# Performance work log

Hardware: AMD Instinct MI355X
Metric: run time of the kernel (lower is better)

The kernel has to match this reference:

```python
import jax, jax.numpy as jnp
import numpy as np

T, B, H, L = 1024, 64, 512, 2
IN = 512  # input_size == hidden_size so layer weights stack
GATE = 3 * H  # fixed-forget subLSTM: in_gate, out_gate, z


def setup_inputs() -> dict:
    key = jax.random.key(0)
    ks = jax.random.split(key, 6)
    stdv = 1.0 / np.sqrt(H)
    u = lambda k, shape: jax.random.uniform(k, shape, jnp.float32, -stdv, stdv)
    return {
        "x": jax.random.normal(ks[0], (T, B, IN), jnp.float32),
        "h0": jnp.zeros((L, B, H), jnp.float32),
        "c0": jnp.zeros((L, B, H), jnp.float32),
        "W": u(ks[1], (L, GATE, IN)),
        "R": u(ks[2], (L, GATE, H)),
        "bi": u(ks[3], (L, GATE)),
        "bh": u(ks[4], (L, GATE)),
        "f": u(ks[5], (L, H)),
    }


def reference(x, h0, c0, W, R, bi, bh, f):
    num_layers = W.shape[0]
    fg = jax.nn.sigmoid(f)  # fixed forget gate per layer/unit, [L, H]

    def step(carry, x_t):
        h, c = carry  # each [L, B, H]
        inp = x_t  # [B, IN]
        new_h, new_c = [], []
        for l in range(num_layers):
            proj = jax.nn.sigmoid(inp @ W[l].T + bi[l] + h[l] @ R[l].T + bh[l])
            i_g, o_g, z = jnp.split(proj, 3, axis=-1)
            c_t = c[l] * fg[l] + z - i_g
            h_t = jax.nn.sigmoid(c_t) - o_g
            new_h.append(h_t)
            new_c.append(c_t)
            inp = h_t
        return (jnp.stack(new_h), jnp.stack(new_c)), inp

    (h_f, c_f), output = jax.lax.scan(step, (h0, c0), x)
    return output, h_f, c_f
```

## Files before the change

kernel.cpp:

```cpp
#include <hip/hip_runtime.h>
#include <hip/hip_bf16.h>
#include <stdint.h>


#define TSTEPS 1024
#define BATCH  64
#define HID    512
#define GATE   1536
#define GROWS  8
#define NT     256
#define NBLOCKS 256

typedef unsigned long long u64;
typedef __attribute__((ext_vector_type(8))) short short8;
typedef __attribute__((ext_vector_type(4))) short short4v;
typedef __attribute__((ext_vector_type(4))) float floatx4;

__device__ __forceinline__ float sigmoidf_(float x) { return 1.0f / (1.0f + __expf(-x)); }

__device__ __forceinline__ unsigned short f2bf(float x) {
    union { float f; unsigned u; } v; v.f = x;
    unsigned r = v.u + 0x7FFFu + ((v.u >> 16) & 1u);
    return (unsigned short)(r >> 16);
}

__device__ __forceinline__ short8 load_frag(const float* p) {
    floatx4 a = *(const floatx4*)p;
    floatx4 b = *(const floatx4*)(p + 4);
    short8 r;
#pragma unroll
    for (int j = 0; j < 4; ++j) { r[j] = (short)f2bf(a[j]); r[j+4] = (short)f2bf(b[j]); }
    return r;
}

__device__ __forceinline__ u64 ring_ld(const u64* p) {
    return __hip_atomic_load(p, __ATOMIC_RELAXED, __HIP_MEMORY_SCOPE_AGENT);
}
__device__ __forceinline__ void ring_st(u64* p, u64 v) {
    __hip_atomic_store(p, v, __ATOMIC_RELAXED, __HIP_MEMORY_SCOPE_AGENT);
}

__global__ __launch_bounds__(256) void xconvert(const float* __restrict__ x,
                                                unsigned short* __restrict__ xb) {
    const size_t i = ((size_t)blockIdx.x*256 + threadIdx.x) * 8;
    floatx4 a = *(const floatx4*)(x + i);
    floatx4 b = *(const floatx4*)(x + i + 4);
    short8 p;
#pragma unroll
    for (int j = 0; j < 4; ++j) { p[j] = (short)f2bf(a[j]); p[j+4] = (short)f2bf(b[j]); }
    *(short8*)(xb + i) = p;
}

__global__ __launch_bounds__(NT, 1) void sublstm_fused(
    const unsigned short* __restrict__ xb,
    const float* __restrict__ W,
    const float* __restrict__ R,
    const float* __restrict__ bi,
    const float* __restrict__ bh,
    const float* __restrict__ fw,
    const float* __restrict__ h0,
    const float* __restrict__ c0,
    u64* __restrict__ ring,
    float* __restrict__ out)
{
    const int tid  = threadIdx.x;
    const int lane = tid & 63;
    const int wid  = tid >> 6;
    const int bid  = blockIdx.x;
    const int g    = bid & 7;
    const int bidx = bid >> 3;
    const int col0 = bidx << 4;

    __shared__ __align__(16) unsigned short x_tile[16][520];
    __shared__ __align__(16) unsigned short hA[16][520];
    __shared__ __align__(16) unsigned short hB[16][520];
    __shared__ float proj[3][16][17];

    for (int i = tid; i < 16*520; i += NT) {
        ((unsigned short*)x_tile)[i] = 0;
        ((unsigned short*)hA)[i] = 0;
        ((unsigned short*)hB)[i] = 0;
    }
    __syncthreads();

    const int lrow = lane & 15;
    const int lk   = (lane >> 4) << 3;

    short8 wf0[16], rf0[16], wf1[16], rf1[16];
    float bias0 = 0.f, bias1 = 0.f;
    if (wid < 3) {
        const int wrow = wid*HID + col0 + lrow;
#pragma unroll
        for (int kc = 0; kc < 16; ++kc) {
            wf0[kc] = load_frag(W + (size_t)wrow*HID + kc*32 + lk);
            rf0[kc] = load_frag(R + (size_t)wrow*HID + kc*32 + lk);
            wf1[kc] = load_frag(W + ((size_t)GATE + wrow)*HID + kc*32 + lk);
            rf1[kc] = load_frag(R + ((size_t)GATE + wrow)*HID + kc*32 + lk);
        }
        bias0 = bi[wrow] + bh[wrow];
        bias1 = bi[GATE + wrow] + bh[GATE + wrow];
    }

    const int lyr  = tid >> 7;
    const int srow = (tid >> 4) & 7;
    const int scol = tid & 15;
    const float fgv = sigmoidf_(fw[(size_t)lyr*HID + col0 + scol]);
    float creg = c0[((size_t)lyr*BATCH + g*GROWS + srow)*HID + col0 + scol];

    {
        const unsigned short* xp = xb + (size_t)g*GROWS*HID;
        for (int w = tid; w < GROWS*HID/8; w += NT) {
            const int r = w >> 6, c8 = (w & 63) << 3;
            *(short8*)(&x_tile[r][c8]) = *(const short8*)(xp + (size_t)r*HID + c8);
        }
        const float* hp0 = h0 + (size_t)g*GROWS*HID;
        const float* hp1 = h0 + ((size_t)BATCH + g*GROWS)*HID;
        for (int w = tid; w < GROWS*HID/4; w += NT) {
            const int r = w >> 7, c4 = (w & 127) << 2;
            floatx4 va_ = *(const floatx4*)(hp0 + (size_t)r*HID + c4);
            floatx4 vb_ = *(const floatx4*)(hp1 + (size_t)r*HID + c4);
            short4v pa, pb;
#pragma unroll
            for (int j = 0; j < 4; ++j) { pa[j] = (short)f2bf(va_[j]); pb[j] = (short)f2bf(vb_[j]); }
            *(short4v*)(&hA[r][c4]) = pa;
            *(short4v*)(&hB[r][c4]) = pb;
        }
    }
    __syncthreads();

    int budget = 1 << 22;
    int pend_t = -1;
    float pend_h = 0.f, pend_c = 0.f;
    u64 va0[8], va1[8];
    short8 xr0, xr1;

    for (int i = 0; i <= TSTEPS; ++i) {
        if (i >= 1) {
            const unsigned want = (unsigned)i;
            const u64* rb0 = ring + ((size_t)((i - 1) & 3)*8 + g)*2048;
            unsigned stale = 0;
#pragma unroll
            for (int k = 0; k < 8; ++k)
                if ((unsigned)(va0[k] >> 32) != want) stale |= (1u << k);
            int pass = 0;
            while (__any((int)(stale != 0)) && budget > 0) {
                if (pass++) __builtin_amdgcn_s_sleep(1);
#pragma unroll
                for (int k = 0; k < 8; ++k)
                    if (stale & (1u << k)) va0[k] = ring_ld(rb0 + tid + (k << 8));
#pragma unroll
                for (int k = 0; k < 8; ++k)
                    if (stale & (1u << k))
                        if ((unsigned)(va0[k] >> 32) == want) stale &= ~(1u << k);
                --budget;
            }
#pragma unroll
            for (int k = 0; k < 8; ++k) {
                const int w = tid + (k << 8);
                const int b = w >> 6, r = (w >> 3) & 7, u = w & 7;
                *(unsigned*)(&hA[r][b*16 + u*2]) = (unsigned)va0[k];
            }
            if (i < TSTEPS) {
                *(short8*)(&x_tile[tid >> 6][(tid & 63) << 3]) = xr0;
                const int w1 = tid + 256;
                *(short8*)(&x_tile[w1 >> 6][(w1 & 63) << 3]) = xr1;
            }
        }
        __syncthreads();

        if (wid < 3 && i < TSTEPS) {
            floatx4 a0a = {0,0,0,0}, a0b = {0,0,0,0};
#pragma unroll
            for (int kc = 0; kc < 16; ++kc) {
                short8 afx = *(const short8*)(&x_tile[lrow][kc*32 + lk]);
                short8 afh = *(const short8*)(&hA[lrow][kc*32 + lk]);
                a0a = __builtin_amdgcn_mfma_f32_16x16x32_bf16(afx, wf0[kc], a0a, 0, 0, 0);
                a0b = __builtin_amdgcn_mfma_f32_16x16x32_bf16(afh, rf0[kc], a0b, 0, 0, 0);
            }
            const int erow0 = (lane >> 4) << 2, ecol = lrow;
#pragma unroll
            for (int q = 0; q < 4; ++q)
                proj[wid][erow0 + q][ecol] = sigmoidf_(a0a[q] + a0b[q] + bias0);
        }
        __syncthreads();

        if (i >= 2) {
            const u64* rb1 = ring + ((size_t)(4 + ((i - 2) & 3))*8 + g)*2048;
#pragma unroll
            for (int k = 0; k < 8; ++k)
                va1[k] = ring_ld(rb1 + tid + (k << 8));
        }
        __builtin_amdgcn_sched_barrier(0);

        if (pend_t >= 0) {
            if (lyr == 1)
                out[((size_t)pend_t*BATCH + g*GROWS + srow)*HID + col0 + scol] = pend_h;
            if (pend_t == TSTEPS - 1) {
                const size_t fo = (size_t)TSTEPS*BATCH*HID
                                + ((size_t)lyr*BATCH + g*GROWS + srow)*HID + col0 + scol;
                out[fo] = pend_h;
                out[fo + (size_t)2*BATCH*HID] = pend_c;
            }
            pend_t = -1;
        }
        if (lyr == 0 && i < TSTEPS) {
            const float ig = proj[0][srow][scol];
            const float og = proj[1][srow][scol];
            const float zz = proj[2][srow][scol];
            const float c_ = creg*fgv + zz - ig;
            creg = c_;
            const float h_ = sigmoidf_(c_) - og;
            const unsigned hu = __float_as_uint(h_);
            const unsigned pu = (unsigned)__builtin_amdgcn_ds_swizzle((int)hu, 0x041F);
            unsigned pay;
            asm volatile("v_cvt_pk_bf16_f32 %0, %1, %2"
                         : "=v"(pay) : "v"(h_), "v"(__uint_as_float(pu)));
            if (!(scol & 1)) {
                const size_t off = (((size_t)(i & 3)*8 + g)*32 + bidx)*64
                                 + srow*8 + (scol >> 1);
                ring_st(ring + off, (u64)pay | ((u64)(unsigned)(i + 1) << 32));
            }
            if (i == TSTEPS - 1) { pend_t = i; pend_h = h_; pend_c = c_; }
        }
        __builtin_amdgcn_sched_barrier(0);

        floatx4 a1a = {0,0,0,0};
        if (wid < 3 && i >= 1) {
#pragma unroll
            for (int kc = 0; kc < 16; ++kc) {
                short8 afh = *(const short8*)(&hA[lrow][kc*32 + lk]);
                a1a = __builtin_amdgcn_mfma_f32_16x16x32_bf16(afh, wf1[kc], a1a, 0, 0, 0);
            }
        }
        __builtin_amdgcn_sched_barrier(0);

        if (i >= 2) {
            const unsigned want = (unsigned)(i - 1);
            const u64* rb1 = ring + ((size_t)(4 + ((i - 2) & 3))*8 + g)*2048;
            unsigned stale = 0;
#pragma unroll
            for (int k = 0; k < 8; ++k)
                if ((unsigned)(va1[k] >> 32) != want) stale |= (1u << k);
            int pass = 0;
            while (__any((int)(stale != 0)) && budget > 0) {
                if (pass++) __builtin_amdgcn_s_sleep(1);
#pragma unroll
                for (int k = 0; k < 8; ++k)
                    if (stale & (1u << k)) va1[k] = ring_ld(rb1 + tid + (k << 8));
#pragma unroll
                for (int k = 0; k < 8; ++k)
                    if (stale & (1u << k))
                        if ((unsigned)(va1[k] >> 32) == want) stale &= ~(1u << k);
                --budget;
            }
#pragma unroll
            for (int k = 0; k < 8; ++k) {
                const int w = tid + (k << 8);
                const int b = w >> 6, r = (w >> 3) & 7, u = w & 7;
                *(unsigned*)(&hB[r][b*16 + u*2]) = (unsigned)va1[k];
            }
        }
        __syncthreads();

        if (wid < 3 && i >= 1) {
            floatx4 a1b = {0,0,0,0};
#pragma unroll
            for (int kc = 0; kc < 16; ++kc) {
                short8 afb = *(const short8*)(&hB[lrow][kc*32 + lk]);
                a1b = __builtin_amdgcn_mfma_f32_16x16x32_bf16(afb, rf1[kc], a1b, 0, 0, 0);
            }
            const int erow0 = (lane >> 4) << 2, ecol = lrow;
#pragma unroll
            for (int q = 0; q < 4; ++q)
                proj[wid][erow0 + q][ecol] = sigmoidf_(a1a[q] + a1b[q] + bias1);
        }
        __syncthreads();

        if (i < TSTEPS) {
            const u64* rb0n = ring + ((size_t)(i & 3)*8 + g)*2048;
#pragma unroll
            for (int k = 0; k < 8; ++k)
                va0[k] = ring_ld(rb0n + tid + (k << 8));
        }
        if (i + 1 < TSTEPS) {
            const unsigned short* xp = xb + ((size_t)(i + 1)*BATCH + g*GROWS)*HID;
            xr0 = *(const short8*)(xp + (size_t)(tid >> 6)*HID + ((tid & 63) << 3));
            const int w1 = tid + 256;
            xr1 = *(const short8*)(xp + (size_t)(w1 >> 6)*HID + ((w1 & 63) << 3));
        }
        __builtin_amdgcn_sched_barrier(0);

        if (lyr == 1 && i >= 1) {
            const int t = i - 1;
            const float ig = proj[0][srow][scol];
            const float og = proj[1][srow][scol];
            const float zz = proj[2][srow][scol];
            const float c_ = creg*fgv + zz - ig;
            creg = c_;
            const float h_ = sigmoidf_(c_) - og;
            const unsigned hu = __float_as_uint(h_);
            const unsigned pu = (unsigned)__builtin_amdgcn_ds_swizzle((int)hu, 0x041F);
            unsigned pay;
            asm volatile("v_cvt_pk_bf16_f32 %0, %1, %2"
                         : "=v"(pay) : "v"(h_), "v"(__uint_as_float(pu)));
            if (!(scol & 1)) {
                const size_t off = (((size_t)(4 + (t & 3))*8 + g)*32 + bidx)*64
                                 + srow*8 + (scol >> 1);
                ring_st(ring + off, (u64)pay | ((u64)(unsigned)(t + 1) << 32));
            }
            pend_t = t; pend_h = h_; pend_c = c_;
        }
    }

    if (pend_t >= 0) {
        if (lyr == 1)
            out[((size_t)pend_t*BATCH + g*GROWS + srow)*HID + col0 + scol] = pend_h;
        if (pend_t == TSTEPS - 1) {
            const size_t fo = (size_t)TSTEPS*BATCH*HID
                            + ((size_t)lyr*BATCH + g*GROWS + srow)*HID + col0 + scol;
            out[fo] = pend_h;
            out[fo + (size_t)2*BATCH*HID] = pend_c;
        }
    }
}

extern "C" void kernel_launch(void* const* d_in, const int* in_sizes, int n_in,
                              void* d_out, int out_size, void* d_ws, size_t ws_size,
                              hipStream_t stream)
{
    (void)in_sizes; (void)n_in; (void)out_size; (void)ws_size;
    const float* x  = (const float*)d_in[0];
    const float* h0 = (const float*)d_in[1];
    const float* c0 = (const float*)d_in[2];
    const float* W  = (const float*)d_in[3];
    const float* R  = (const float*)d_in[4];
    const float* bi = (const float*)d_in[5];
    const float* bh = (const float*)d_in[6];
    const float* fw = (const float*)d_in[7];
    float* out = (float*)d_out;

    u64* ring = (u64*)d_ws;
    unsigned short* xbuf = (unsigned short*)((char*)d_ws + (2u << 20));

    hipMemsetAsync(d_ws, 0, (size_t)2*4*8*2048*8, stream);

    xconvert<<<dim3(TSTEPS*BATCH*HID/(256*8)), dim3(256), 0, stream>>>(x, xbuf);

    sublstm_fused<<<dim3(NBLOCKS), dim3(NT), 0, stream>>>(
        xbuf, W, R, bi, bh, fw, h0, c0, ring, out);
}
```

Measured before the change: 3.467 ms.

## Precompute next-step input projection off the critical path and split MFMA accumulators

The layer-0 input projection x_t·W is now computed one step ahead, at the end of the previous iteration, and kept in registers, so the recurrent critical section only runs the h·R MFMAs. The x tile is prefetched two steps ahead. The recurrent MFMA chains are split into two independent accumulators to hide MFMA dependency latency. Output stores and ring loads are moved into slack between barriers. This adds register pressure and reorders the x_tile writes relative to barriers, which could race if the sync placement is wrong.

```diff
diff --git a/kernel.cpp b/kernel.cpp
--- a/kernel.cpp
+++ b/kernel.cpp
@@ -128,11 +128,26 @@
     }
     __syncthreads();
 
+    floatx4 a0a_sav = {0,0,0,0};
+    if (wid < 3) {
+#pragma unroll
+        for (int kc = 0; kc < 16; ++kc) {
+            short8 afx = *(const short8*)(&x_tile[lrow][kc*32 + lk]);
+            a0a_sav = __builtin_amdgcn_mfma_f32_16x16x32_bf16(afx, wf0[kc], a0a_sav, 0, 0, 0);
+        }
+    }
+    short8 xr0, xr1;
+    {
+        const unsigned short* xp = xb + (size_t)BATCH*HID + (size_t)g*GROWS*HID;
+        xr0 = *(const short8*)(xp + (size_t)(tid >> 6)*HID + ((tid & 63) << 3));
+        const int w1 = tid + 256;
+        xr1 = *(const short8*)(xp + (size_t)(w1 >> 6)*HID + ((w1 & 63) << 3));
+    }
+
     int budget = 1 << 22;
     int pend_t = -1;
     float pend_h = 0.f, pend_c = 0.f;
     u64 va0[8], va1[8];
-    short8 xr0, xr1;
 
     for (int i = 0; i <= TSTEPS; ++i) {
         if (i >= 1) {
@@ -160,27 +175,22 @@
                 const int b = w >> 6, r = (w >> 3) & 7, u = w & 7;
                 *(unsigned*)(&hA[r][b*16 + u*2]) = (unsigned)va0[k];
             }
-            if (i < TSTEPS) {
-                *(short8*)(&x_tile[tid >> 6][(tid & 63) << 3]) = xr0;
-                const int w1 = tid + 256;
-                *(short8*)(&x_tile[w1 >> 6][(w1 & 63) << 3]) = xr1;
-            }
         }
         __syncthreads();
 
         if (wid < 3 && i < TSTEPS) {
-            floatx4 a0a = {0,0,0,0}, a0b = {0,0,0,0};
-#pragma unroll
-            for (int kc = 0; kc < 16; ++kc) {
-                short8 afx = *(const short8*)(&x_tile[lrow][kc*32 + lk]);
-                short8 afh = *(const short8*)(&hA[lrow][kc*32 + lk]);
-                a0a = __builtin_amdgcn_mfma_f32_16x16x32_bf16(afx, wf0[kc], a0a, 0, 0, 0);
-                a0b = __builtin_amdgcn_mfma_f32_16x16x32_bf16(afh, rf0[kc], a0b, 0, 0, 0);
+            floatx4 ae = {0,0,0,0}, ao = {0,0,0,0};
+#pragma unroll
+            for (int kc = 0; kc < 16; kc += 2) {
+                short8 h0f = *(const short8*)(&hA[lrow][kc*32 + lk]);
+                short8 h1f = *(const short8*)(&hA[lrow][(kc+1)*32 + lk]);
+                ae = __builtin_amdgcn_mfma_f32_16x16x32_bf16(h0f, rf0[kc],   ae, 0, 0, 0);
+                ao = __builtin_amdgcn_mfma_f32_16x16x32_bf16(h1f, rf0[kc+1], ao, 0, 0, 0);
             }
             const int erow0 = (lane >> 4) << 2, ecol = lrow;
 #pragma unroll
             for (int q = 0; q < 4; ++q)
-                proj[wid][erow0 + q][ecol] = sigmoidf_(a0a[q] + a0b[q] + bias0);
+                proj[wid][erow0 + q][ecol] = sigmoidf_(a0a_sav[q] + ae[q] + ao[q] + bias0);
         }
         __syncthreads();
 
@@ -192,17 +202,6 @@
         }
         __builtin_amdgcn_sched_barrier(0);
 
-        if (pend_t >= 0) {
-            if (lyr == 1)
-                out[((size_t)pend_t*BATCH + g*GROWS + srow)*HID + col0 + scol] = pend_h;
-            if (pend_t == TSTEPS - 1) {
-                const size_t fo = (size_t)TSTEPS*BATCH*HID
-                                + ((size_t)lyr*BATCH + g*GROWS + srow)*HID + col0 + scol;
-                out[fo] = pend_h;
-                out[fo + (size_t)2*BATCH*HID] = pend_c;
-            }
-            pend_t = -1;
-        }
         if (lyr == 0 && i < TSTEPS) {
             const float ig = proj[0][srow][scol];
             const float og = proj[1][srow][scol];
@@ -260,35 +259,51 @@
                 *(unsigned*)(&hB[r][b*16 + u*2]) = (unsigned)va1[k];
             }
         }
-        __syncthreads();
-
-        if (wid < 3 && i >= 1) {
-            floatx4 a1b = {0,0,0,0};
-#pragma unroll
-            for (int kc = 0; kc < 16; ++kc) {
-                short8 afb = *(const short8*)(&hB[lrow][kc*32 + lk]);
-                a1b = __builtin_amdgcn_mfma_f32_16x16x32_bf16(afb, rf1[kc], a1b, 0, 0, 0);
-            }
-            const int erow0 = (lane >> 4) << 2, ecol = lrow;
-#pragma unroll
-            for (int q = 0; q < 4; ++q)
-                proj[wid][erow0 + q][ecol] = sigmoidf_(a1a[q] + a1b[q] + bias1);
-        }
-        __syncthreads();
-
-        if (i < TSTEPS) {
-            const u64* rb0n = ring + ((size_t)(i & 3)*8 + g)*2048;
-#pragma unroll
-            for (int k = 0; k < 8; ++k)
-                va0[k] = ring_ld(rb0n + tid + (k << 8));
-        }
         if (i + 1 < TSTEPS) {
-            const unsigned short* xp = xb + ((size_t)(i + 1)*BATCH + g*GROWS)*HID;
+            *(short8*)(&x_tile[tid >> 6][(tid & 63) << 3]) = xr0;
+            const int w1 = tid + 256;
+            *(short8*)(&x_tile[w1 >> 6][(w1 & 63) << 3]) = xr1;
+        }
+        if (i + 2 < TSTEPS) {
+            const unsigned short* xp = xb + ((size_t)(i + 2)*BATCH + g*GROWS)*HID;
             xr0 = *(const short8*)(xp + (size_t)(tid >> 6)*HID + ((tid & 63) << 3));
             const int w1 = tid + 256;
             xr1 = *(const short8*)(xp + (size_t)(w1 >> 6)*HID + ((w1 & 63) << 3));
         }
-        __builtin_amdgcn_sched_barrier(0);
+        if (pend_t >= 0) {
+            if (lyr == 1)
+                out[((size_t)pend_t*BATCH + g*GROWS + srow)*HID + col0 + scol] = pend_h;
+            if (pend_t == TSTEPS - 1) {
+                const size_t fo = (size_t)TSTEPS*BATCH*HID
+                                + ((size_t)lyr*BATCH + g*GROWS + srow)*HID + col0 + scol;
+                out[fo] = pend_h;
+                out[fo + (size_t)2*BATCH*HID] = pend_c;
+            }
+            pend_t = -1;
+        }
+        __syncthreads();
+
+        if (wid < 3 && i >= 1) {
+            floatx4 be = {0,0,0,0}, bo = {0,0,0,0};
+#pragma unroll
+            for (int kc = 0; kc < 16; kc += 2) {
+                short8 b0f = *(const short8*)(&hB[lrow][kc*32 + lk]);
+                short8 b1f = *(const short8*)(&hB[lrow][(kc+1)*32 + lk]);
+                be = __builtin_amdgcn_mfma_f32_16x16x32_bf16(b0f, rf1[kc],   be, 0, 0, 0);
+                bo = __builtin_amdgcn_mfma_f32_16x16x32_bf16(b1f, rf1[kc+1], bo, 0, 0, 0);
+            }
+            const int erow0 = (lane >> 4) << 2, ecol = lrow;
+#pragma unroll
+            for (int q = 0; q < 4; ++q)
+                proj[wid][erow0 + q][ecol] = sigmoidf_(a1a[q] + be[q] + bo[q] + bias1);
+        }
+        if (i < TSTEPS) {
+            const u64* rb0n = ring + ((size_t)(i & 3)*8 + g)*2048;
+#pragma unroll
+            for (int k = 0; k < 8; ++k)
+                va0[k] = ring_ld(rb0n + tid + (k << 8));
+        }
+        __syncthreads();
 
         if (lyr == 1 && i >= 1) {
             const int t = i - 1;
@@ -310,6 +325,16 @@
             }
             pend_t = t; pend_h = h_; pend_c = c_;
         }
+
+        if (wid < 3 && i + 1 < TSTEPS) {
+            floatx4 an = {0,0,0,0};
+#pragma unroll
+            for (int kc = 0; kc < 16; ++kc) {
+                short8 afx = *(const short8*)(&x_tile[lrow][kc*32 + lk]);
+                an = __builtin_amdgcn_mfma_f32_16x16x32_bf16(afx, wf0[kc], an, 0, 0, 0);
+            }
+            a0a_sav = an;
+        }
     }
 
     if (pend_t >= 0) {
```

Measured after the change: 3.429 ms. No clear change (-1.1%).

## Halve block count with 32 columns per block and six MFMA waves

Applied to the files above, without the earlier changes.

Each block now owns 32 hidden columns instead of 16 and runs six waves, all of which do MFMA work, instead of four waves with one idle. This halves the number of persistent blocks, so fewer producers write to the ring buffer and the per-step barriers cover fewer participants. The layer-1 ring reload and the output stores are moved to overlap with other work, and x-prefetch now happens earlier. In exchange each block carries more weight fragments in registers and does more elementwise work, which lengthens the serial per-step path inside a block.

```diff
diff --git a/kernel.cpp b/kernel.cpp
--- a/kernel.cpp
+++ b/kernel.cpp
@@ -8,8 +8,10 @@
 #define HID    512
 #define GATE   1536
 #define GROWS  8
-#define NT     256
-#define NBLOCKS 256
+#define NT     384
+#define NBLOCKS 128
+#define BPG    16
+#define GWORDS 2048
 
 typedef unsigned long long u64;
 typedef __attribute__((ext_vector_type(8))) short short8;
@@ -69,12 +71,12 @@
     const int bid  = blockIdx.x;
     const int g    = bid & 7;
     const int bidx = bid >> 3;
-    const int col0 = bidx << 4;
+    const int col0 = bidx << 5;
 
     __shared__ __align__(16) unsigned short x_tile[16][520];
     __shared__ __align__(16) unsigned short hA[16][520];
     __shared__ __align__(16) unsigned short hB[16][520];
-    __shared__ float proj[3][16][17];
+    __shared__ float proj[3][16][33];
 
     for (int i = tid; i < 16*520; i += NT) {
         ((unsigned short*)x_tile)[i] = 0;
@@ -88,8 +90,8 @@
 
     short8 wf0[16], rf0[16], wf1[16], rf1[16];
     float bias0 = 0.f, bias1 = 0.f;
-    if (wid < 3) {
-        const int wrow = wid*HID + col0 + lrow;
+    {
+        const int wrow = (wid >> 1)*HID + col0 + (wid & 1)*16 + lrow;
 #pragma unroll
         for (int kc = 0; kc < 16; ++kc) {
             wf0[kc] = load_frag(W + (size_t)wrow*HID + kc*32 + lk);
@@ -101,11 +103,20 @@
         bias1 = bi[GATE + wrow] + bh[GATE + wrow];
     }
 
-    const int lyr  = tid >> 7;
-    const int srow = (tid >> 4) & 7;
-    const int scol = tid & 15;
-    const float fgv = sigmoidf_(fw[(size_t)lyr*HID + col0 + scol]);
-    float creg = c0[((size_t)lyr*BATCH + g*GROWS + srow)*HID + col0 + scol];
+    const bool hasL0 = (tid < 256);
+    const bool hasL1 = (tid >= 128);
+    const int c0i = tid, c1i = tid - 128;
+    const int sr0 = (c0i >> 5) & 7, sc0 = c0i & 31;
+    const int sr1 = (c1i >> 5) & 7, sc1 = c1i & 31;
+    float fgv0 = 0.f, fgv1 = 0.f, creg0 = 0.f, creg1 = 0.f;
+    if (hasL0) {
+        fgv0 = sigmoidf_(fw[col0 + sc0]);
+        creg0 = c0[((size_t)g*GROWS + sr0)*HID + col0 + sc0];
+    }
+    if (hasL1) {
+        fgv1 = sigmoidf_(fw[(size_t)HID + col0 + sc1]);
+        creg1 = c0[((size_t)BATCH + g*GROWS + sr1)*HID + col0 + sc1];
+    }
 
     {
         const unsigned short* xp = xb + (size_t)g*GROWS*HID;
@@ -131,44 +142,66 @@
     int budget = 1 << 22;
     int pend_t = -1;
     float pend_h = 0.f, pend_c = 0.f;
-    u64 va0[8], va1[8];
+    u64 va0[6], va1[6];
     short8 xr0, xr1;
+    {
+        const unsigned short* xp = xb + (size_t)BATCH*HID + (size_t)g*GROWS*HID;
+        xr0 = *(const short8*)(xp + (size_t)(tid >> 6)*HID + ((tid & 63) << 3));
+        if (tid < 128) {
+            const int w1 = tid + NT;
+            xr1 = *(const short8*)(xp + (size_t)(w1 >> 6)*HID + ((w1 & 63) << 3));
+        }
+    }
 
     for (int i = 0; i <= TSTEPS; ++i) {
         if (i >= 1) {
             const unsigned want = (unsigned)i;
-            const u64* rb0 = ring + ((size_t)((i - 1) & 3)*8 + g)*2048;
+            const u64* rb0 = ring + ((size_t)((i - 1) & 3)*8 + g)*GWORDS;
             unsigned stale = 0;
 #pragma unroll
-            for (int k = 0; k < 8; ++k)
-                if ((unsigned)(va0[k] >> 32) != want) stale |= (1u << k);
+            for (int k = 0; k < 6; ++k) {
+                const int w = tid + k*NT;
+                if (w < GWORDS && (unsigned)(va0[k] >> 32) != want) stale |= (1u << k);
+            }
             int pass = 0;
             while (__any((int)(stale != 0)) && budget > 0) {
                 if (pass++) __builtin_amdgcn_s_sleep(1);
 #pragma unroll
-                for (int k = 0; k < 8; ++k)
-                    if (stale & (1u << k)) va0[k] = ring_ld(rb0 + tid + (k << 8));
-#pragma unroll
-                for (int k = 0; k < 8; ++k)
+                for (int k = 0; k < 6; ++k)
+                    if (stale & (1u << k)) va0[k] = ring_ld(rb0 + tid + k*NT);
+#pragma unroll
+                for (int k = 0; k < 6; ++k)
                     if (stale & (1u << k))
                         if ((unsigned)(va0[k] >> 32) == want) stale &= ~(1u << k);
                 --budget;
             }
 #pragma unroll
-            for (int k = 0; k < 8; ++k) {
-                const int w = tid + (k << 8);
-                const int b = w >> 6, r = (w >> 3) & 7, u = w & 7;
-                *(unsigned*)(&hA[r][b*16 + u*2]) = (unsigned)va0[k];
+            for (int k = 0; k < 6; ++k) {
+                const int w = tid + k*NT;
+                if (w < GWORDS) {
+                    const int b = w >> 7, r = (w >> 4) & 7, u = w & 15;
+                    *(unsigned*)(&hA[r][b*32 + u*2]) = (unsigned)va0[k];
+                }
             }
             if (i < TSTEPS) {
                 *(short8*)(&x_tile[tid >> 6][(tid & 63) << 3]) = xr0;
-                const int w1 = tid + 256;
-                *(short8*)(&x_tile[w1 >> 6][(w1 & 63) << 3]) = xr1;
+                if (tid < 128) {
+                    const int w1 = tid + NT;
+                    *(short8*)(&x_tile[w1 >> 6][(w1 & 63) << 3]) = xr1;
+                }
+            }
+        }
+        if (i + 1 < TSTEPS) {
+            const unsigned short* xp = xb + ((size_t)(i + 1)*BATCH + g*GROWS)*HID;
+            xr0 = *(const short8*)(xp + (size_t)(tid >> 6)*HID + ((tid & 63) << 3));
+            if (tid < 128) {
+                const int w1 = tid + NT;
+                xr1 = *(const short8*)(xp + (size_t)(w1 >> 6)*HID + ((w1 & 63) << 3));
             }
         }
         __syncthreads();
 
-        if (wid < 3 && i < TSTEPS) {
+        if (i < TSTEPS) {
             floatx4 a0a = {0,0,0,0}, a0b = {0,0,0,0};
 #pragma unroll
             for (int kc = 0; kc < 16; ++kc) {
@@ -177,55 +210,51 @@
                 a0a = __builtin_amdgcn_mfma_f32_16x16x32_bf16(afx, wf0[kc], a0a, 0, 0, 0);
                 a0b = __builtin_amdgcn_mfma_f32_16x16x32_bf16(afh, rf0[kc], a0b, 0, 0, 0);
             }
-            const int erow0 = (lane >> 4) << 2, ecol = lrow;
+            const int erow0 = (lane >> 4) << 2, ecol = (wid & 1)*16 + lrow;
 #pragma unroll
             for (int q = 0; q < 4; ++q)
-                proj[wid][erow0 + q][ecol] = sigmoidf_(a0a[q] + a0b[q] + bias0);
+                proj[wid >> 1][erow0 + q][ecol] = sigmoidf_(a0a[q] + a0b[q] + bias0);
         }
         __syncthreads();
 
         if (i >= 2) {
-            const u64* rb1 = ring + ((size_t)(4 + ((i - 2) & 3))*8 + g)*2048;
-#pragma unroll
-            for (int k = 0; k < 8; ++k)
-                va1[k] = ring_ld(rb1 + tid + (k << 8));
+            const u64* rb1 = ring + (size_t)4*8*GWORDS + ((size_t)((i - 2) & 3)*8 + g)*GWORDS;
+#pragma unroll
+            for (int k = 0; k < 6; ++k) {
+                const int w = tid + k*NT;
+                if (w < GWORDS) va1[k] = ring_ld(rb1 + w);
+            }
         }
         __builtin_amdgcn_sched_barrier(0);
 
-        if (pend_t >= 0) {
-            if (lyr == 1)
-                out[((size_t)pend_t*BATCH + g*GROWS + srow)*HID + col0 + scol] = pend_h;
-            if (pend_t == TSTEPS - 1) {
-                const size_t fo = (size_t)TSTEPS*BATCH*HID
-                                + ((size_t)lyr*BATCH + g*GROWS + srow)*HID + col0 + scol;
-                out[fo] = pend_h;
-                out[fo + (size_t)2*BATCH*HID] = pend_c;
-            }
-            pend_t = -1;
-        }
-        if (lyr == 0 && i < TSTEPS) {
-            const float ig = proj[0][srow][scol];
-            const float og = proj[1][srow][scol];
-            const float zz = proj[2][srow][scol];
-            const float c_ = creg*fgv + zz - ig;
-            creg = c_;
+        if (hasL0 && i < TSTEPS) {
+            const float ig = proj[0][sr0][sc0];
+            const float og = proj[1][sr0][sc0];
+            const float zz = proj[2][sr0][sc0];
+            const float c_ = creg0*fgv0 + zz - ig;
+            creg0 = c_;
             const float h_ = sigmoidf_(c_) - og;
             const unsigned hu = __float_as_uint(h_);
             const unsigned pu = (unsigned)__builtin_amdgcn_ds_swizzle((int)hu, 0x041F);
             unsigned pay;
             asm volatile("v_cvt_pk_bf16_f32 %0, %1, %2"
                          : "=v"(pay) : "v"(h_), "v"(__uint_as_float(pu)));
-            if (!(scol & 1)) {
-                const size_t off = (((size_t)(i & 3)*8 + g)*32 + bidx)*64
-                                 + srow*8 + (scol >> 1);
+            if (!(sc0 & 1)) {
+                const size_t off = (((size_t)(i & 3)*8 + g)*BPG + bidx)*128
+                                 + sr0*16 + (sc0 >> 1);
                 ring_st(ring + off, (u64)pay | ((u64)(unsigned)(i + 1) << 32));
             }
-            if (i == TSTEPS - 1) { pend_t = i; pend_h = h_; pend_c = c_; }
+            if (i == TSTEPS - 1) {
+                const size_t fo = (size_t)TSTEPS*BATCH*HID
+                                + ((size_t)g*GROWS + sr0)*HID + col0 + sc0;
+                out[fo] = h_;
+                out[fo + (size_t)2*BATCH*HID] = creg0;
+            }
         }
         __builtin_amdgcn_sched_barrier(0);
 
         floatx4 a1a = {0,0,0,0};
-        if (wid < 3 && i >= 1) {
+        if (i >= 1) {
 #pragma unroll
             for (int kc = 0; kc < 16; ++kc) {
                 short8 afh = *(const short8*)(&hA[lrow][kc*32 + lk]);
@@ -236,76 +265,85 @@
 
         if (i >= 2) {
             const unsigned want = (unsigned)(i - 1);
-            const u64* rb1 = ring + ((size_t)(4 + ((i - 2) & 3))*8 + g)*2048;
+            const u64* rb1 = ring + (size_t)4*8*GWORDS + ((size_t)((i - 2) & 3)*8 + g)*GWORDS;
             unsigned stale = 0;
 #pragma unroll
-            for (int k = 0; k < 8; ++k)
-                if ((unsigned)(va1[k] >> 32) != want) stale |= (1u << k);
+            for (int k = 0; k < 6; ++k) {
+                const int w = tid + k*NT;
+                if (w < GWORDS && (unsigned)(va1[k] >> 32) != want) stale |= (1u << k);
+            }
             int pass = 0;
             while (__any((int)(stale != 0)) && budget > 0) {
                 if (pass++) __builtin_amdgcn_s_sleep(1);
 #pragma unroll
-                for (int k = 0; k < 8; ++k)
-                    if (stale & (1u << k)) va1[k] = ring_ld(rb1 + tid + (k << 8));
-#pragma unroll
-                for (int k = 0; k < 8; ++k)
+                for (int k = 0; k < 6; ++k)
+                    if (stale & (1u << k)) va1[k] = ring_ld(rb1 + tid + k*NT);
+#pragma unroll
+                for (int k = 0; k < 6; ++k)
                     if (stale & (1u << k))
                         if ((unsigned)(va1[k] >> 32) == want) stale &= ~(1u << k);
                 --budget;
             }
 #pragma unroll
-            for (int k = 0; k < 8; ++k) {
-                const int w = tid + (k << 8);
-                const int b = w >> 6, r = (w >> 3) & 7, u = w & 7;
-                *(unsigned*)(&hB[r][b*16 + u*2]) = (unsigned)va1[k];
-            }
+            for (int k = 0; k < 6; ++k) {
+                const int w = tid + k*NT;
+                if (w < GWORDS) {
+                    const int b = w >> 7, r = (w >> 4) & 7, u = w & 15;
+                    *(unsigned*)(&hB[r][b*32 + u*2]) = (unsigned)va1[k];
+                }
+            }
+        }
+        if (pend_t >= 0) {
+            out[((size_t)pend_t*BATCH + g*GROWS + sr1)*HID + col0 + sc1] = pend_h;
+            if (pend_t == TSTEPS - 1) {
+                const size_t fo = (size_t)TSTEPS*BATCH*HID
+                                + ((size_t)BATCH + g*GROWS + sr1)*HID + col0 + sc1;
+                out[fo] = pend_h;
+                out[fo + (size_t)2*BATCH*HID] = pend_c;
+            }
+            pend_t = -1;
         }
         __syncthreads();
 
-        if (wid < 3 && i >= 1) {
+        if (i >= 1) {
             floatx4 a1b = {0,0,0,0};
 #pragma unroll
             for (int kc = 0; kc < 16; ++kc) {
                 short8 afb = *(const short8*)(&hB[lrow][kc*32 + lk]);
                 a1b = __builtin_amdgcn_mfma_f32_16x16x32_bf16(afb, rf1[kc], a1b, 0, 0, 0);
             }
-            const int erow0 = (lane >> 4) << 2, ecol = lrow;
+            const int erow0 = (lane >> 4) << 2, ecol = (wid & 1)*16 + lrow;
 #pragma unroll
             for (int q = 0; q < 4; ++q)
-                proj[wid][erow0 + q][ecol] = sigmoidf_(a1a[q] + a1b[q] + bias1);
+                proj[wid >> 1][erow0 + q][ecol] = sigmoidf_(a1a[q] + a1b[q] + bias1);
+        }
+        if (i < TSTEPS) {
+            const u64* rb0n = ring + ((size_t)(i & 3)*8 + g)*GWORDS;
+#pragma unroll
+            for (int k = 0; k < 6; ++k) {
+                const int w = tid + k*NT;
+                if (w < GWORDS) va0[k] = ring_ld(rb0n + w);
+            }
         }
         __syncthreads();
 
-        if (i < TSTEPS) {
-            const u64* rb0n = ring + ((size_t)(i & 3)*8 + g)*2048;
-#pragma unroll
-            for (int k = 0; k < 8; ++k)
-                va0[k] = ring_ld(rb0n + tid + (k << 8));
-        }
-        if (i + 1 < TSTEPS) {
-            const unsigned short* xp = xb + ((size_t)(i + 1)*BATCH + g*GROWS)*HID;
-            xr0 = *(const short8*)(xp + (size_t)(tid >> 6)*HID + ((tid & 63) << 3));
-            const int w1 = tid + 256;
-            xr1 = *(const short8*)(xp + (size_t)(w1 >> 6)*HID + ((w1 & 63) << 3));
-        }
-        __builtin_amdgcn_sched_barrier(0);
-
-        if (lyr == 1 && i >= 1) {
+        if (hasL1 && i >= 1) {
             const int t = i - 1;
-            const float ig = proj[0][srow][scol];
-            const float og = proj[1][srow][scol];
-            const float zz = proj[2][srow][scol];
-            const float c_ = creg*fgv + zz - ig;
-            creg = c_;
+            const float ig = proj[0][sr1][sc1];
+            const float og = proj[1][sr1][sc1];
+            const float zz = proj[2][sr1][sc1];
+            const float c_ = creg1*fgv1 + zz - ig;
+            creg1 = c_;
             const float h_ = sigmoidf_(c_) - og;
             const unsigned hu = __float_as_uint(h_);
             const unsigned pu = (unsigned)__builtin_amdgcn_ds_swizzle((int)hu, 0x041F);
             unsigned pay;
             asm volatile("v_cvt_pk_bf16_f32 %0, %1, %2"
                          : "=v"(pay) : "v"(h_), "v"(__uint_as_float(pu)));
-            if (!(scol & 1)) {
-                const size_t off = (((size_t)(4 + (t & 3))*8 + g)*32 + bidx)*64
-                                 + srow*8 + (scol >> 1);
+            if (!(sc1 & 1)) {
+                const size_t off = (size_t)4*8*GWORDS
+                                 + (((size_t)(t & 3)*8 + g)*BPG + bidx)*128
+                                 + sr1*16 + (sc1 >> 1);
                 ring_st(ring + off, (u64)pay | ((u64)(unsigned)(t + 1) << 32));
             }
             pend_t = t; pend_h = h_; pend_c = c_;
@@ -313,11 +351,10 @@
     }
 
     if (pend_t >= 0) {
-        if (lyr == 1)
-            out[((size_t)pend_t*BATCH + g*GROWS + srow)*HID + col0 + scol] = pend_h;
+        out[((size_t)pend_t*BATCH + g*GROWS + sr1)*HID + col0 + sc1] = pend_h;
         if (pend_t == TSTEPS - 1) {
             const size_t fo = (size_t)TSTEPS*BATCH*HID
-                            + ((size_t)lyr*BATCH + g*GROWS + srow)*HID + col0 + scol;
+                            + ((size_t)BATCH + g*GROWS + sr1)*HID + col0 + sc1;
             out[fo] = pend_h;
             out[fo + (size_t)2*BATCH*HID] = pend_c;
         }
@@ -342,7 +379,7 @@
     u64* ring = (u64*)d_ws;
     unsigned short* xbuf = (unsigned short*)((char*)d_ws + (2u << 20));
 
-    hipMemsetAsync(d_ws, 0, (size_t)2*4*8*2048*8, stream);
+    hipMemsetAsync(d_ws, 0, (size_t)2*4*8*GWORDS*8, stream);
 
     xconvert<<<dim3(TSTEPS*BATCH*HID/(256*8)), dim3(256), 0, stream>>>(x, xbuf);
 
```

Measured after the change: 12.70 ms. +266.1%, slower.
